# Kernel tuning notes

Hardware: AMD Instinct MI355X
Metric: run time of the kernel (lower is better)

## Reference

```python
import jax, jax.numpy as jnp
import numpy as np

E = 128   # embedding_dim
H = 8     # num_attention_heads
D = 16    # head_size = E // H


def setup_inputs() -> dict:
    key = jax.random.key(0)
    ks = jax.random.split(key, 7)
    B, N = 2, 512
    x = jax.random.normal(ks[0], (B, N, E), jnp.float32)
    e = jax.random.uniform(ks[1], (B, N, N), jnp.float32)  # dense pairwise edge weights
    s_qkv = 1.0 / np.sqrt(D)
    w_qkv = jax.random.uniform(ks[2], (3 * H * D, E), jnp.float32, -s_qkv, s_qkv)
    w_ekv = jax.random.normal(ks[3], (2 * H * D, 1), jnp.float32) * 1.0
    b_ekv = jax.random.normal(ks[4], (2 * H * D,), jnp.float32) * 0.01
    s_prj = 1.0 / np.sqrt(E)
    w_prj = jax.random.uniform(ks[5], (E, H * D), jnp.float32, -s_prj, s_prj)
    b_prj = jnp.zeros((E,), jnp.float32)
    return {"x": x, "e": e, "w_qkv": w_qkv, "w_ekv": w_ekv,
            "b_ekv": b_ekv, "w_prj": w_prj, "b_prj": b_prj}


def reference(x, e, w_qkv, w_ekv, b_ekv, w_prj, b_prj):
    B, N, _ = x.shape
    # qkv projection: [B,N,3*H*D] split per einops '(S H D)'
    qkv = (x @ w_qkv.T).reshape(B, N, 3, H, D)
    q = jnp.transpose(qkv[:, :, 0], (0, 2, 1, 3))  # [B,H,N,D]
    k = jnp.transpose(qkv[:, :, 1], (0, 2, 1, 3))  # [B,H,N,D]
    v = jnp.transpose(qkv[:, :, 2], (0, 2, 1, 3))  # [B,H,N,D]
    # edge-conditioned K/V biases: Linear(1 -> 2HD) + LeakyReLU(0.01)
    ekv = jax.nn.leaky_relu(e[..., None] * w_ekv[:, 0] + b_ekv)  # [B,N,M,2HD]
    ekv = ekv.reshape(B, N, N, 2, H, D)
    ekm = jnp.transpose(ekv[..., 0, :, :], (0, 3, 1, 2, 4))  # [B,H,N,M,D]
    evm = jnp.transpose(ekv[..., 1, :, :], (0, 3, 1, 2, 4))  # [B,H,N,M,D]
    # dots[b,h,n,m] = q[b,h,n] . (k[b,h,n] + ekm[b,h,n,m])
    # NOTE: original uses the key of the *query* node n (broadcast over m).
    dots = jnp.sum(q * k, axis=-1)[..., None] \
        + jnp.einsum('bhnd,bhnmd->bhnm', q, ekm)
    attn = jax.nn.softmax(dots / np.sqrt(D), axis=-1)  # [B,H,N,M]
    # hat[b,h,n] = sum_m attn * (v[b,h,n] + evm[b,h,n,m])
    hat = v * jnp.sum(attn, axis=-1)[..., None] \
        + jnp.einsum('bhnm,bhnmd->bhnd', attn, evm)  # [B,H,N,D]
    out = jnp.transpose(hat, (0, 2, 1, 3)).reshape(B, N, H * D) @ w_prj.T + b_prj
    return out
```

## Files before the change

### kernel.cpp

```cpp
#include <hip/hip_runtime.h>
#include <math.h>

#define BATCH 2
#define NSEQ  512
#define EDIM  128
#define HNUM  8
#define DDIM  16
#define MROWS (BATCH*NSEQ)

template<int BM, int BN, int TM, int TN>
__global__ __launch_bounds__(256)
void gemm_tn(const float* __restrict__ A, const float* __restrict__ B,
             const float* __restrict__ bias, float* __restrict__ C,
             int M, int N) {
    constexpr int K  = 128;
    constexpr int KP = K + 1;
    __shared__ float As[BM][KP];
    __shared__ float Bs[BN][KP];

    const int tid  = threadIdx.x;
    const int row0 = blockIdx.y * BM;
    const int col0 = blockIdx.x * BN;

    #pragma unroll
    for (int it = 0; it < (BM * 32) / 256; ++it) {
        int idx = tid + it * 256;
        int r = idx >> 5, c4 = idx & 31;
        float4 v = *(const float4*)(A + (size_t)(row0 + r) * K + c4 * 4);
        As[r][c4*4+0] = v.x; As[r][c4*4+1] = v.y;
        As[r][c4*4+2] = v.z; As[r][c4*4+3] = v.w;
    }
    #pragma unroll
    for (int it = 0; it < (BN * 32) / 256; ++it) {
        int idx = tid + it * 256;
        int r = idx >> 5, c4 = idx & 31;
        float4 v = *(const float4*)(B + (size_t)(col0 + r) * K + c4 * 4);
        Bs[r][c4*4+0] = v.x; Bs[r][c4*4+1] = v.y;
        Bs[r][c4*4+2] = v.z; Bs[r][c4*4+3] = v.w;
    }
    __syncthreads();

    const int tx = tid & 15;
    const int ty = tid >> 4;
    float acc[TM][TN] = {};

    for (int kk = 0; kk < K; ++kk) {
        float a[TM], b[TN];
        #pragma unroll
        for (int i = 0; i < TM; ++i) a[i] = As[ty*TM + i][kk];
        #pragma unroll
        for (int j = 0; j < TN; ++j) b[j] = Bs[tx*TN + j][kk];
        #pragma unroll
        for (int i = 0; i < TM; ++i)
            #pragma unroll
            for (int j = 0; j < TN; ++j)
                acc[i][j] = fmaf(a[i], b[j], acc[i][j]);
    }

    #pragma unroll
    for (int i = 0; i < TM; ++i) {
        int r = row0 + ty*TM + i;
        #pragma unroll
        for (int j = 0; j < TN; ++j) {
            int cc = col0 + tx*TN + j;
            float v = acc[i][j];
            if (bias) v += bias[cc];
            C[(size_t)r * N + cc] = v;
        }
    }
}

__global__ __launch_bounds__(256)
void attn_kernel(const float* __restrict__ qkv, const float* __restrict__ e,
                 const float* __restrict__ wekv, const float* __restrict__ bekv,
                 float* __restrict__ hat) {
    const int lane = threadIdx.x & 63;
    const int wv   = threadIdx.x >> 6;
    const int idx  = blockIdx.x * 4 + wv;
    const int h    = idx & (HNUM - 1);
    const int bn   = idx >> 3;

    const float* qrow = qkv + (size_t)bn * (3 * EDIM) + h * DDIM;
    const float* krow = qrow + EDIM;
    const float* vrow = qrow + 2 * EDIM;
    const float* erow = e + (size_t)bn * NSEQ;

    float q[DDIM], wk[DDIM], bk[DDIM];
    float qk = 0.f;
    #pragma unroll
    for (int d = 0; d < DDIM; ++d) {
        q[d]  = qrow[d];
        qk    = fmaf(q[d], krow[d], qk);
        wk[d] = wekv[h * DDIM + d];
        bk[d] = bekv[h * DDIM + d];
    }

    const float SC = 0.25f * 1.44269504088896340736f;

    float dots[NSEQ / 64], ev[NSEQ / 64];
    float lmax = -1e30f;
    #pragma unroll
    for (int c = 0; c < NSEQ / 64; ++c) {
        float s = erow[c * 64 + lane];
        ev[c] = s;
        float dot = qk;
        #pragma unroll
        for (int d = 0; d < DDIM; ++d) {
            float t = fmaf(s, wk[d], bk[d]);
            t = fmaxf(t, 0.01f * t);
            dot = fmaf(q[d], t, dot);
        }
        dot *= SC;
        dots[c] = dot;
        lmax = fmaxf(lmax, dot);
    }
    #pragma unroll
    for (int off = 32; off >= 1; off >>= 1)
        lmax = fmaxf(lmax, __shfl_xor(lmax, off, 64));

    float wvv[DDIM], bv[DDIM], acc[DDIM];
    #pragma unroll
    for (int d = 0; d < DDIM; ++d) {
        wvv[d] = wekv[EDIM + h * DDIM + d];
        bv[d]  = bekv[EDIM + h * DDIM + d];
        acc[d] = 0.f;
    }
    float sp = 0.f;
    #pragma unroll
    for (int c = 0; c < NSEQ / 64; ++c) {
        float p = __builtin_exp2f(dots[c] - lmax);
        sp += p;
        float s = ev[c];
        #pragma unroll
        for (int d = 0; d < DDIM; ++d) {
            float t = fmaf(s, wvv[d], bv[d]);
            t = fmaxf(t, 0.01f * t);
            acc[d] = fmaf(p, t, acc[d]);
        }
    }

    #pragma unroll
    for (int off = 1; off < 64; off <<= 1) {
        sp += __shfl_xor(sp, off, 64);
        #pragma unroll
        for (int d = 0; d < DDIM; ++d)
            acc[d] += __shfl_xor(acc[d], off, 64);
    }

    float a = acc[0];
    #pragma unroll
    for (int d = 1; d < DDIM; ++d) a = (lane == d) ? acc[d] : a;
    if (lane < DDIM) {
        float o = vrow[lane] + a / sp;
        hat[(size_t)bn * EDIM + h * DDIM + lane] = o;
    }
}

extern "C" void kernel_launch(void* const* d_in, const int* in_sizes, int n_in,
                              void* d_out, int out_size, void* d_ws, size_t ws_size,
                              hipStream_t stream) {
    const float* x     = (const float*)d_in[0];
    const float* e     = (const float*)d_in[1];
    const float* w_qkv = (const float*)d_in[2];
    const float* w_ekv = (const float*)d_in[3];
    const float* b_ekv = (const float*)d_in[4];
    const float* w_prj = (const float*)d_in[5];
    const float* b_prj = (const float*)d_in[6];
    float* out = (float*)d_out;

    float* qkv = (float*)d_ws;
    float* hat = qkv + (size_t)MROWS * 3 * EDIM;

    gemm_tn<32, 64, 2, 4><<<dim3(384 / 64, MROWS / 32), 256, 0, stream>>>(
        x, w_qkv, nullptr, qkv, MROWS, 3 * EDIM);

    attn_kernel<<<(BATCH * NSEQ * HNUM) / 4, 256, 0, stream>>>(
        qkv, e, w_ekv, b_ekv, hat);

    gemm_tn<32, 32, 2, 2><<<dim3(128 / 32, MROWS / 32), 256, 0, stream>>>(
        hat, w_prj, b_prj, out, MROWS, EDIM);
}
```

Measured before the change: 93.84 us.

## Fuse output projection into attention, swizzle QKV GEMM, rewrite LeakyReLU via abs

Replaces the generic GEMM with a specialized QKV GEMM that stores float4 tiles in shared memory with an XOR swizzle and writes vectorized outputs. The attention kernel now runs one block per query row with all eight heads and performs the output projection in-block from shared memory, which drops the third launch and the hat round-trip through global memory. LeakyReLU is rewritten as 0.505*t + 0.495*|t|, so the linear part is folded into per-row scalars (q·w, q·b, and p·s sums) and the inner loops need only one FMA plus abs per element. It also switches to the hardware exp2 intrinsic. In exchange each block redoes the w_prj dot products per row, and there are fewer, larger blocks.

After: 94.11 us. Within noise of the previous version (+0.3%).

```diff
diff --git a/kernel.cpp b/kernel.cpp
--- a/kernel.cpp
+++ b/kernel.cpp
@@ -8,94 +8,101 @@
 #define DDIM  16
 #define MROWS (BATCH*NSEQ)
 
-template<int BM, int BN, int TM, int TN>
 __global__ __launch_bounds__(256)
-void gemm_tn(const float* __restrict__ A, const float* __restrict__ B,
-             const float* __restrict__ bias, float* __restrict__ C,
-             int M, int N) {
-    constexpr int K  = 128;
-    constexpr int KP = K + 1;
-    __shared__ float As[BM][KP];
-    __shared__ float Bs[BN][KP];
+void qkv_gemm(const float* __restrict__ x, const float* __restrict__ w,
+              float* __restrict__ qkv) {
+    __shared__ float4 As[32 * 32];
+    __shared__ float4 Bs[64 * 32];
 
     const int tid  = threadIdx.x;
-    const int row0 = blockIdx.y * BM;
-    const int col0 = blockIdx.x * BN;
-
-    #pragma unroll
-    for (int it = 0; it < (BM * 32) / 256; ++it) {
+    const int row0 = blockIdx.y * 32;
+    const int col0 = blockIdx.x * 64;
+
+    #pragma unroll
+    for (int it = 0; it < 4; ++it) {
         int idx = tid + it * 256;
-        int r = idx >> 5, c4 = idx & 31;
-        float4 v = *(const float4*)(A + (size_t)(row0 + r) * K + c4 * 4);
-        As[r][c4*4+0] = v.x; As[r][c4*4+1] = v.y;
-        As[r][c4*4+2] = v.z; As[r][c4*4+3] = v.w;
-    }
-    #pragma unroll
-    for (int it = 0; it < (BN * 32) / 256; ++it) {
+        int r = idx >> 5, k4 = idx & 31;
+        As[r * 32 + (k4 ^ ((r >> 2) & 7))] =
+            ((const float4*)(x + (size_t)(row0 + r) * 128))[k4];
+    }
+    #pragma unroll
+    for (int it = 0; it < 8; ++it) {
         int idx = tid + it * 256;
-        int r = idx >> 5, c4 = idx & 31;
-        float4 v = *(const float4*)(B + (size_t)(col0 + r) * K + c4 * 4);
-        Bs[r][c4*4+0] = v.x; Bs[r][c4*4+1] = v.y;
-        Bs[r][c4*4+2] = v.z; Bs[r][c4*4+3] = v.w;
+        int r = idx >> 5, k4 = idx & 31;
+        Bs[r * 32 + (k4 ^ ((r >> 2) & 7))] =
+            ((const float4*)(w + (size_t)(col0 + r) * 128))[k4];
     }
     __syncthreads();
 
+    const int ty = tid >> 4;
     const int tx = tid & 15;
-    const int ty = tid >> 4;
-    float acc[TM][TN] = {};
-
-    for (int kk = 0; kk < K; ++kk) {
-        float a[TM], b[TN];
-        #pragma unroll
-        for (int i = 0; i < TM; ++i) a[i] = As[ty*TM + i][kk];
-        #pragma unroll
-        for (int j = 0; j < TN; ++j) b[j] = Bs[tx*TN + j][kk];
-        #pragma unroll
-        for (int i = 0; i < TM; ++i)
-            #pragma unroll
-            for (int j = 0; j < TN; ++j)
-                acc[i][j] = fmaf(a[i], b[j], acc[i][j]);
-    }
-
-    #pragma unroll
-    for (int i = 0; i < TM; ++i) {
-        int r = row0 + ty*TM + i;
-        #pragma unroll
-        for (int j = 0; j < TN; ++j) {
-            int cc = col0 + tx*TN + j;
-            float v = acc[i][j];
-            if (bias) v += bias[cc];
-            C[(size_t)r * N + cc] = v;
+    const int ra  = ty * 2;
+    const int swa = (ra >> 2) & 7;
+    const int rb  = tx * 4;
+    const int swb = tx & 7;
+
+    float acc[2][4] = {};
+    #pragma unroll
+    for (int k4 = 0; k4 < 32; ++k4) {
+        float4 a0 = As[ ra      * 32 + (k4 ^ swa)];
+        float4 a1 = As[(ra + 1) * 32 + (k4 ^ swa)];
+        float4 bv[4];
+        #pragma unroll
+        for (int j = 0; j < 4; ++j)
+            bv[j] = Bs[(rb + j) * 32 + (k4 ^ swb)];
+        #pragma unroll
+        for (int j = 0; j < 4; ++j) {
+            acc[0][j] = fmaf(a0.x, bv[j].x, acc[0][j]);
+            acc[0][j] = fmaf(a0.y, bv[j].y, acc[0][j]);
+            acc[0][j] = fmaf(a0.z, bv[j].z, acc[0][j]);
+            acc[0][j] = fmaf(a0.w, bv[j].w, acc[0][j]);
+            acc[1][j] = fmaf(a1.x, bv[j].x, acc[1][j]);
+            acc[1][j] = fmaf(a1.y, bv[j].y, acc[1][j]);
+            acc[1][j] = fmaf(a1.z, bv[j].z, acc[1][j]);
+            acc[1][j] = fmaf(a1.w, bv[j].w, acc[1][j]);
         }
     }
+
+    #pragma unroll
+    for (int i = 0; i < 2; ++i) {
+        float* crow = qkv + (size_t)(row0 + ra + i) * 384 + col0 + rb;
+        *(float4*)crow = make_float4(acc[i][0], acc[i][1], acc[i][2], acc[i][3]);
+    }
 }
 
-__global__ __launch_bounds__(256)
-void attn_kernel(const float* __restrict__ qkv, const float* __restrict__ e,
-                 const float* __restrict__ wekv, const float* __restrict__ bekv,
-                 float* __restrict__ hat) {
-    const int lane = threadIdx.x & 63;
-    const int wv   = threadIdx.x >> 6;
-    const int idx  = blockIdx.x * 4 + wv;
-    const int h    = idx & (HNUM - 1);
-    const int bn   = idx >> 3;
-
-    const float* qrow = qkv + (size_t)bn * (3 * EDIM) + h * DDIM;
+__global__ __launch_bounds__(512)
+void attn_proj(const float* __restrict__ qkv, const float* __restrict__ e,
+               const float* __restrict__ wekv, const float* __restrict__ bekv,
+               const float* __restrict__ wprj, const float* __restrict__ bprj,
+               float* __restrict__ out) {
+    __shared__ float hat_s[EDIM];
+
+    const int tid  = threadIdx.x;
+    const int lane = tid & 63;
+    const int h    = tid >> 6;
+    const int bn   = blockIdx.x;
+
+    const float* qrow = qkv + (size_t)bn * 384 + h * DDIM;
     const float* krow = qrow + EDIM;
     const float* vrow = qrow + 2 * EDIM;
     const float* erow = e + (size_t)bn * NSEQ;
 
-    float q[DDIM], wk[DDIM], bk[DDIM];
-    float qk = 0.f;
+    const float SC = 0.25f * 1.44269504088896340736f;
+
+    float wk[DDIM], bk[DDIM], cd[DDIM];
+    float qk = 0.f, qwk = 0.f, qbk = 0.f;
     #pragma unroll
     for (int d = 0; d < DDIM; ++d) {
-        q[d]  = qrow[d];
-        qk    = fmaf(q[d], krow[d], qk);
+        float q = qrow[d];
+        qk  = fmaf(q, krow[d], qk);
         wk[d] = wekv[h * DDIM + d];
         bk[d] = bekv[h * DDIM + d];
-    }
-
-    const float SC = 0.25f * 1.44269504088896340736f;
+        qwk = fmaf(q, wk[d], qwk);
+        qbk = fmaf(q, bk[d], qbk);
+        cd[d] = 0.495f * SC * q;
+    }
+    const float Alin = SC * 0.505f * qwk;
+    const float base = SC * (qk + 0.505f * qbk);
 
     float dots[NSEQ / 64], ev[NSEQ / 64];
     float lmax = -1e30f;
@@ -103,14 +110,12 @@
     for (int c = 0; c < NSEQ / 64; ++c) {
         float s = erow[c * 64 + lane];
         ev[c] = s;
-        float dot = qk;
+        float dot = fmaf(s, Alin, base);
         #pragma unroll
         for (int d = 0; d < DDIM; ++d) {
             float t = fmaf(s, wk[d], bk[d]);
-            t = fmaxf(t, 0.01f * t);
-            dot = fmaf(q[d], t, dot);
+            dot = fmaf(cd[d], fabsf(t), dot);
         }
-        dot *= SC;
         dots[c] = dot;
         lmax = fmaxf(lmax, dot);
     }
@@ -118,42 +123,65 @@
     for (int off = 32; off >= 1; off >>= 1)
         lmax = fmaxf(lmax, __shfl_xor(lmax, off, 64));
 
-    float wvv[DDIM], bv[DDIM], acc[DDIM];
+    float wvv[DDIM], bv[DDIM], racc[DDIM];
     #pragma unroll
     for (int d = 0; d < DDIM; ++d) {
-        wvv[d] = wekv[EDIM + h * DDIM + d];
-        bv[d]  = bekv[EDIM + h * DDIM + d];
-        acc[d] = 0.f;
-    }
-    float sp = 0.f;
+        wvv[d]  = wekv[EDIM + h * DDIM + d];
+        bv[d]   = bekv[EDIM + h * DDIM + d];
+        racc[d] = 0.f;
+    }
+    float sp = 0.f, spe = 0.f;
     #pragma unroll
     for (int c = 0; c < NSEQ / 64; ++c) {
-        float p = __builtin_exp2f(dots[c] - lmax);
-        sp += p;
+        float p = __builtin_amdgcn_exp2f(dots[c] - lmax);
         float s = ev[c];
+        sp  += p;
+        spe  = fmaf(p, s, spe);
+        float pm = 0.495f * p;
         #pragma unroll
         for (int d = 0; d < DDIM; ++d) {
             float t = fmaf(s, wvv[d], bv[d]);
-            t = fmaxf(t, 0.01f * t);
-            acc[d] = fmaf(p, t, acc[d]);
+            racc[d] = fmaf(pm, fabsf(t), racc[d]);
         }
     }
 
     #pragma unroll
     for (int off = 1; off < 64; off <<= 1) {
-        sp += __shfl_xor(sp, off, 64);
+        sp  += __shfl_xor(sp,  off, 64);
+        spe += __shfl_xor(spe, off, 64);
         #pragma unroll
         for (int d = 0; d < DDIM; ++d)
-            acc[d] += __shfl_xor(acc[d], off, 64);
-    }
-
-    float a = acc[0];
-    #pragma unroll
-    for (int d = 1; d < DDIM; ++d) a = (lane == d) ? acc[d] : a;
+            racc[d] += __shfl_xor(racc[d], off, 64);
+    }
+
+    float rsel = racc[0];
+    #pragma unroll
+    for (int d = 1; d < DDIM; ++d) rsel = (lane == d) ? racc[d] : rsel;
     if (lane < DDIM) {
-        float o = vrow[lane] + a / sp;
-        hat[(size_t)bn * EDIM + h * DDIM + lane] = o;
-    }
+        float wvs = wekv[EDIM + h * DDIM + lane];
+        float bvs = bekv[EDIM + h * DDIM + lane];
+        float acc = rsel + 0.505f * (fmaf(wvs, spe, bvs * sp));
+        hat_s[h * DDIM + lane] = vrow[lane] + acc / sp;
+    }
+    __syncthreads();
+
+    const int c    = tid >> 2;
+    const int quad = tid & 3;
+    const float4* wp = (const float4*)(wprj + (size_t)c * EDIM + quad * 32);
+    const float4* hp = (const float4*)(hat_s + quad * 32);
+    float s = 0.f;
+    #pragma unroll
+    for (int j = 0; j < 8; ++j) {
+        float4 wv4 = wp[j], hv4 = hp[j];
+        s = fmaf(wv4.x, hv4.x, s);
+        s = fmaf(wv4.y, hv4.y, s);
+        s = fmaf(wv4.z, hv4.z, s);
+        s = fmaf(wv4.w, hv4.w, s);
+    }
+    s += __shfl_xor(s, 1, 64);
+    s += __shfl_xor(s, 2, 64);
+    if (quad == 0)
+        out[(size_t)bn * EDIM + c] = s + bprj[c];
 }
 
 extern "C" void kernel_launch(void* const* d_in, const int* in_sizes, int n_in,
@@ -169,14 +197,8 @@
     float* out = (float*)d_out;
 
     float* qkv = (float*)d_ws;
-    float* hat = qkv + (size_t)MROWS * 3 * EDIM;
-
-    gemm_tn<32, 64, 2, 4><<<dim3(384 / 64, MROWS / 32), 256, 0, stream>>>(
-        x, w_qkv, nullptr, qkv, MROWS, 3 * EDIM);
-
-    attn_kernel<<<(BATCH * NSEQ * HNUM) / 4, 256, 0, stream>>>(
-        qkv, e, w_ekv, b_ekv, hat);
-
-    gemm_tn<32, 32, 2, 2><<<dim3(128 / 32, MROWS / 32), 256, 0, stream>>>(
-        hat, w_prj, b_prj, out, MROWS, EDIM);
+
+    qkv_gemm<<<dim3(384 / 64, MROWS / 32), 256, 0, stream>>>(x, w_qkv, qkv);
+
+    attn_proj<<<MROWS, 512, 0, stream>>>(qkv, e, w_ekv, b_ekv, w_prj, b_prj, out);
 }
```
